# Optimization experiments

Hardware: AMD Instinct MI355X
Metric: run time of the kernel (lower is better)

## Reference

```python
import jax, jax.numpy as jnp
import numpy as np


def setup_inputs() -> dict:
    key = jax.random.key(0)
    k1, k2 = jax.random.split(key)
    B, S, H, D = 4, 2048, 12, 64
    v = jax.random.normal(k1, (B, S, H, D), dtype=jnp.float32)
    # learned per-head positional weights, sorted ascending along last dim
    # (mirrors torch.sort(torch.randn(H, S), dim=-1)[0])
    w = jnp.sort(jax.random.normal(k2, (H, S), dtype=jnp.float32), axis=-1)
    return {"v": v, "w": w}


def reference(v, w):
    # PositionalBias._naive
    # v: [B, S, H, D]; w: [H, S_max]
    B, S, H, D = v.shape
    seq_len = S - 2  # v[:, 1:-1] is the non-special-token span
    w_ = w[:, :seq_len]  # [H, seq_len]
    # _construct_bias builds bias[h, l, j] = w[h, |l - j|] (symmetric Toeplitz)
    pos = jnp.arange(seq_len)
    idx = jnp.abs(pos[:, None] - pos[None, :])  # [seq_len, seq_len]
    bias = w_[:, idx]  # [H, seq_len, seq_len]
    # zero-pad one row/col on each side -> [H, S, S]
    bias = jnp.pad(bias, ((0, 0), (1, 1), (1, 1)))
    # z_pb: [1, S, H]
    z_pb = jnp.sum(bias, axis=-1).T[None, :, :]
    # pbv: [B, S, H, D]
    pbv = jnp.einsum('nlhd,hlj->njhd', v, bias)
    return (pbv, z_pb)
```

## Files before the change

### kernel.cpp

```cpp
#include <hip/hip_runtime.h>
#include <hip/hip_bf16.h>


typedef short short8 __attribute__((ext_vector_type(8)));
typedef float floatx4 __attribute__((ext_vector_type(4)));
typedef unsigned uint4_ __attribute__((ext_vector_type(4)));

#define QN 4352

__device__ __attribute__((aligned(16))) short g_vt[4 * 12 * 64 * 2048];
__device__ __attribute__((aligned(16))) short g_wt[12 * QN * 8];

__device__ __forceinline__ unsigned short f2bf(float f) {
  union { __hip_bfloat16 b; unsigned short u; } cv;
  cv.b = __float2bfloat16(f);
  return cv.u;
}

__global__ __launch_bounds__(256) void prep_kernel(const float* __restrict__ v,
                                                   const float* __restrict__ w,
                                                   float* __restrict__ out) {
  __shared__ unsigned tls[64 * 65];
  __shared__ float zls[4096];
  __shared__ float wsum[4];

  const int bx  = blockIdx.x;
  const int tid = threadIdx.x;

  if (bx >= 780) {
    const int idx = bx - 780;
    const int h = idx >> 4;
    const int c = idx & 15;
    const float* wh = w + (size_t)h * 2048;
    short* F = g_wt + (size_t)h * QN * 8;
    const int qs = c * 272;
    for (int q = qs + tid; q < qs + 272; q += 256) {
      unsigned short buf[8] __attribute__((aligned(16)));
      #pragma unroll
      for (int i = 0; i < 8; ++i) {
        int t = 2174 - q - i;
        int a = t < 0 ? -t : t;
        buf[i] = (a <= 2045) ? f2bf(wh[a]) : (unsigned short)0;
      }
      *(short8*)&F[(size_t)q * 8] = *(const short8*)buf;
    }
    return;
  }

  if (bx >= 768) {
    const int h = bx - 768;
    float* wvv = zls;
    float* pfx = zls + 2048;
    const float* wh = w + (size_t)h * 2048;
    float* zout = out + 6291456;
    for (int i = tid; i < 2048; i += 256) wvv[i] = (i < 2046) ? wh[i] : 0.f;
    __syncthreads();
    const int base = tid * 8;
    float run0 = 0.f;
    #pragma unroll
    for (int k = 0; k < 8; ++k) run0 += wvv[base + k];
    float x = run0;
    #pragma unroll
    for (int dd = 1; dd < 64; dd <<= 1) {
      float y = __shfl_up(x, dd);
      if ((tid & 63) >= dd) x += y;
    }
    if ((tid & 63) == 63) wsum[tid >> 6] = x;
    __syncthreads();
    const int wid4 = tid >> 6;
    float woff = 0.f;
    #pragma unroll
    for (int u = 0; u < 3; ++u) { float t = wsum[u]; if (u < wid4) woff += t; }
    float pr = x + woff - run0;
    #pragma unroll
    for (int k = 0; k < 8; ++k) { pr += wvv[base + k]; pfx[base + k] = pr; }
    __syncthreads();
    for (int i = tid; i < 2046; i += 256) {
      float z = pfx[i] + pfx[2045 - i] - wvv[0];
      zout[(size_t)(i + 1) * 12 + h] = z;
    }
    if (tid == 0) { zout[h] = 0.f; zout[(size_t)2047 * 12 + h] = 0.f; }
    return;
  }

  const int chunk = bx & 15;
  const int slice = bx >> 4;
  const int n = slice / 12, h = slice - n * 12;
  const int lane = tid & 63;
  const int wv   = tid >> 6;
  const int lbase = chunk * 128 + wv * 32;

  const float* src = v + (((size_t)n * 2048 + lbase) * 12 + h) * 64 + lane;
  #pragma unroll
  for (int kk = 0; kk < 16; ++kk) {
    float f0 = src[(size_t)(2 * kk)     * 768];
    float f1 = src[(size_t)(2 * kk + 1) * 768];
    int l = lbase + 2 * kk;
    unsigned lo = (l == 0)        ? 0u : (unsigned)f2bf(f0);
    unsigned hi = (l + 1 == 2047) ? 0u : (unsigned)f2bf(f1);
    tls[lane * 65 + wv * 16 + kk] = lo | (hi << 16);
  }
  __syncthreads();

  const int r = tid >> 2;
  const int m = tid & 3;
  unsigned xbuf[16];
  #pragma unroll
  for (int k = 0; k < 16; ++k) xbuf[k] = tls[r * 65 + m * 16 + k];
  unsigned* dstu = (unsigned*)(g_vt + (((size_t)n * 12 + h) * 64 + r) * 2048 +
                               (size_t)chunk * 128) + m * 16;
  #pragma unroll
  for (int k4 = 0; k4 < 4; ++k4) {
    uint4_ val = {xbuf[k4 * 4], xbuf[k4 * 4 + 1], xbuf[k4 * 4 + 2], xbuf[k4 * 4 + 3]};
    *(uint4_*)&dstu[k4 * 4] = val;
  }
}

__global__ __launch_bounds__(256, 3) void gemm_kernel(float* __restrict__ out) {
  __shared__ __attribute__((aligned(16))) short Als[2304 * 8];

  const int bx  = blockIdx.x;
  const int tid = threadIdx.x;

  const int slice = bx % 48;
  const int jt    = bx / 48;
  const int ndt = slice & 3;
  const int h   = slice >> 2;
  const int lane = tid & 63;
  const int wid  = tid >> 6;
  const int lm = lane & 15, quad = lane >> 4;
  const int jb = jt * 128;
  const int d  = wid * 16 + lm;

  const short* vtb = g_vt + (((size_t)ndt * 12 + h) * 64 + d) * 2048;

  short8 afr[16];
  short8 Bp0[4], Bp1[4];

  Bp0[0] = *(const short8*)&vtb[quad * 8];
  Bp1[0] = *(const short8*)&vtb[quad * 8 + 32];
  Bp0[1] = *(const short8*)&vtb[64 + quad * 8];
  Bp1[1] = *(const short8*)&vtb[64 + quad * 8 + 32];

  const short* wsrc = g_wt + (size_t)h * QN * 8 + (size_t)(2047 - jb) * 8;
  #pragma unroll
  for (int k = 0; k < 9; ++k) {
    *(short8*)&Als[(size_t)(k * 256 + tid) * 8] =
        *(const short8*)&wsrc[(size_t)(k * 256 + tid) * 8];
  }
  __syncthreads();

  const int abase = 127 + quad * 8 - lm;
  unsigned az0 = (unsigned)(unsigned long long)(&Als[0]) + (unsigned)(abase * 16) - 1792u;
  unsigned long long vb0 = (unsigned long long)(const void*)(vtb + quad * 8);

  floatx4 acc[8];
  #pragma unroll
  for (int ma = 0; ma < 8; ++ma) acc[ma] = (floatx4){0.f, 0.f, 0.f, 0.f};

#define A_PRO(D) \
  asm volatile("ds_read_b128 %0, %1 offset:%2" : "=v"(afr[D]) : "v"(az0), "n"(256 * (D)));
  A_PRO(0) A_PRO(1) A_PRO(2) A_PRO(3) A_PRO(4)
  A_PRO(5) A_PRO(6) A_PRO(7) A_PRO(8) A_PRO(9)
#undef A_PRO

#define G_ITER(T)                                                                        \
  {                                                                                      \
    if ((T) < 30) {                                                                      \
      asm volatile("global_load_dwordx4 %0, %1, off offset:%2"                           \
                   : "=v"(Bp0[((T) + 2) & 3])                                            \
                   : "v"(vb0), "n"((((T) < 30 ? (T) + 2 : 0) * 128)));                   \
      asm volatile("global_load_dwordx4 %0, %1, off offset:%2"                           \
                   : "=v"(Bp1[((T) + 2) & 3])                                            \
                   : "v"(vb0), "n"((((T) < 30 ? (T) + 2 : 0) * 128 + 64)));              \
    }                                                                                    \
    if ((T) < 31) {                                                                      \
      asm volatile("ds_read_b128 %0, %1 offset:%2"                                       \
                   : "=v"(afr[(4 * (T) + 10) & 15])                                      \
                   : "v"(az0), "n"(((T) < 31 ? 1024 * (T) + 2560 : 0)));                 \
      asm volatile("ds_read_b128 %0, %1 offset:%2"                                       \
                   : "=v"(afr[(4 * (T) + 11) & 15])                                      \
                   : "v"(az0), "n"(((T) < 31 ? 1024 * (T) + 2816 : 0)));                 \
      asm volatile("ds_read_b128 %0, %1 offset:%2"                                       \
                   : "=v"(afr[(4 * (T) + 12) & 15])                                      \
                   : "v"(az0), "n"(((T) < 31 ? 1024 * (T) + 3072 : 0)));                 \
      asm volatile("ds_read_b128 %0, %1 offset:%2"                                       \
                   : "=v"(afr[(4 * (T) + 13) & 15])                                      \
                   : "v"(az0), "n"(((T) < 31 ? 1024 * (T) + 3328 : 0)));                 \
    }                                                                                    \
    if ((T) < 30)       asm volatile("s_waitcnt vmcnt(4) lgkmcnt(4)" ::: "memory");      \
    else if ((T) == 30) asm volatile("s_waitcnt vmcnt(2) lgkmcnt(4)" ::: "memory");      \
    else                asm volatile("s_waitcnt vmcnt(0) lgkmcnt(0)" ::: "memory");      \
    __builtin_amdgcn_sched_barrier(0);                                                   \
    __builtin_amdgcn_s_setprio(1);                                                       \
    _Pragma("unroll")                                                                    \
    for (int ma = 0; ma < 8; ++ma)                         \
      acc[ma] = __builtin_amdgcn_mfma_f32_16x16x32_bf16(                                 \
          afr[(4 * (T) + 7 - ma) & 15], Bp0[(T) & 3], acc[ma], 0, 0, 0);                 \
    _Pragma("unroll")                                                                    \
    for (int ma = 0; ma < 8; ++ma)                        \
      acc[ma] = __builtin_amdgcn_mfma_f32_16x16x32_bf16(                                 \
          afr[(4 * (T) + 9 - ma) & 15], Bp1[(T) & 3], acc[ma], 0, 0, 0);                 \
    __builtin_amdgcn_s_setprio(0);                                                       \
  }

  G_ITER(0)  G_ITER(1)  G_ITER(2)  G_ITER(3)  G_ITER(4)  G_ITER(5)  G_ITER(6)  G_ITER(7)
  G_ITER(8)  G_ITER(9)  G_ITER(10) G_ITER(11) G_ITER(12) G_ITER(13) G_ITER(14) G_ITER(15)
  G_ITER(16) G_ITER(17) G_ITER(18) G_ITER(19) G_ITER(20) G_ITER(21) G_ITER(22) G_ITER(23)
  G_ITER(24) G_ITER(25) G_ITER(26) G_ITER(27) G_ITER(28) G_ITER(29) G_ITER(30) G_ITER(31)
#undef G_ITER

  float* obase = out + (size_t)ndt * 1572864 + (size_t)h * 64 + d;
  #pragma unroll
  for (int ma = 0; ma < 8; ++ma) {
    floatx4 cc = acc[ma];
    #pragma unroll
    for (int r = 0; r < 4; ++r) {
      int j = jb + ma * 16 + quad * 4 + r;
      float val = (j == 0 || j == 2047) ? 0.f : cc[r];
      obase[(size_t)j * 768] = val;
    }
  }
}

extern "C" void kernel_launch(void* const* d_in, const int* in_sizes, int n_in,
                              void* d_out, int out_size, void* d_ws, size_t ws_size,
                              hipStream_t stream) {
  const float* v = (const float*)d_in[0];
  const float* w = (const float*)d_in[1];
  float* out = (float*)d_out;
  prep_kernel<<<dim3(972), 256, 0, stream>>>(v, w, out);
  gemm_kernel<<<dim3(768), 256, 0, stream>>>(out);
}
```

Measured before the change: 106.7 us.

## Fuse prep and GEMM into one kernel with atomic-counter dependency waits

Merges the transpose/bf16-convert, Toeplitz weight-table build and z_pb prefix-sum stages into the GEMM kernel. Each block does its share of prep work, then spins on global atomic counters until the v-transpose slice and the weight table for its head are complete. The point is to drop the second launch and the gap between kernels, and to let prep overlap with GEMM. In exchange it adds spin-wait synchronisation that relies on all 768 blocks being co-resident (checked via an occupancy query, with the two-kernel path as fallback). It also adds counter-reset logic that must be correct across repeated calls.

```diff
diff --git a/kernel.cpp b/kernel.cpp
--- a/kernel.cpp
+++ b/kernel.cpp
@@ -10,6 +10,10 @@
 
 __device__ __attribute__((aligned(16))) short g_vt[4 * 12 * 64 * 2048];
 __device__ __attribute__((aligned(16))) short g_wt[12 * QN * 8];
+__device__ int vt_cnt[48];
+__device__ int wt_cnt[12];
+__device__ int vt_done[48];
+__device__ int wt_done[12];
 
 __device__ __forceinline__ unsigned short f2bf(float f) {
   union { __hip_bfloat16 b; unsigned short u; } cv;
@@ -17,72 +21,26 @@
   return cv.u;
 }
 
-__global__ __launch_bounds__(256) void prep_kernel(const float* __restrict__ v,
-                                                   const float* __restrict__ w,
-                                                   float* __restrict__ out) {
-  __shared__ unsigned tls[64 * 65];
-  __shared__ float zls[4096];
-  __shared__ float wsum[4];
-
-  const int bx  = blockIdx.x;
-  const int tid = threadIdx.x;
-
-  if (bx >= 780) {
-    const int idx = bx - 780;
-    const int h = idx >> 4;
-    const int c = idx & 15;
-    const float* wh = w + (size_t)h * 2048;
-    short* F = g_wt + (size_t)h * QN * 8;
-    const int qs = c * 272;
-    for (int q = qs + tid; q < qs + 272; q += 256) {
-      unsigned short buf[8] __attribute__((aligned(16)));
-      #pragma unroll
-      for (int i = 0; i < 8; ++i) {
-        int t = 2174 - q - i;
-        int a = t < 0 ? -t : t;
-        buf[i] = (a <= 2045) ? f2bf(wh[a]) : (unsigned short)0;
-      }
-      *(short8*)&F[(size_t)q * 8] = *(const short8*)buf;
+__device__ __forceinline__ void do_gwt(int idx, int tid, const float* __restrict__ w) {
+  const int h = idx >> 4;
+  const int c = idx & 15;
+  const float* wh = w + (size_t)h * 2048;
+  short* F = g_wt + (size_t)h * QN * 8;
+  const int qs = c * 272;
+  for (int q = qs + tid; q < qs + 272; q += 256) {
+    unsigned short buf[8] __attribute__((aligned(16)));
+    #pragma unroll
+    for (int i = 0; i < 8; ++i) {
+      int t = 2174 - q - i;
+      int a = t < 0 ? -t : t;
+      buf[i] = (a <= 2045) ? f2bf(wh[a]) : (unsigned short)0;
     }
-    return;
-  }
-
-  if (bx >= 768) {
-    const int h = bx - 768;
-    float* wvv = zls;
-    float* pfx = zls + 2048;
-    const float* wh = w + (size_t)h * 2048;
-    float* zout = out + 6291456;
-    for (int i = tid; i < 2048; i += 256) wvv[i] = (i < 2046) ? wh[i] : 0.f;
-    __syncthreads();
-    const int base = tid * 8;
-    float run0 = 0.f;
-    #pragma unroll
-    for (int k = 0; k < 8; ++k) run0 += wvv[base + k];
-    float x = run0;
-    #pragma unroll
-    for (int dd = 1; dd < 64; dd <<= 1) {
-      float y = __shfl_up(x, dd);
-      if ((tid & 63) >= dd) x += y;
-    }
-    if ((tid & 63) == 63) wsum[tid >> 6] = x;
-    __syncthreads();
-    const int wid4 = tid >> 6;
-    float woff = 0.f;
-    #pragma unroll
-    for (int u = 0; u < 3; ++u) { float t = wsum[u]; if (u < wid4) woff += t; }
-    float pr = x + woff - run0;
-    #pragma unroll
-    for (int k = 0; k < 8; ++k) { pr += wvv[base + k]; pfx[base + k] = pr; }
-    __syncthreads();
-    for (int i = tid; i < 2046; i += 256) {
-      float z = pfx[i] + pfx[2045 - i] - wvv[0];
-      zout[(size_t)(i + 1) * 12 + h] = z;
-    }
-    if (tid == 0) { zout[h] = 0.f; zout[(size_t)2047 * 12 + h] = 0.f; }
-    return;
-  }
-
+    *(short8*)&F[(size_t)q * 8] = *(const short8*)buf;
+  }
+}
+
+__device__ __forceinline__ void do_transpose(int bx, int tid, unsigned* tls,
+                                             const float* __restrict__ v) {
   const int chunk = bx & 15;
   const int slice = bx >> 4;
   const int n = slice / 12, h = slice - n * 12;
@@ -116,12 +74,43 @@
   }
 }
 
-__global__ __launch_bounds__(256, 3) void gemm_kernel(float* __restrict__ out) {
-  __shared__ __attribute__((aligned(16))) short Als[2304 * 8];
-
-  const int bx  = blockIdx.x;
-  const int tid = threadIdx.x;
-
+__device__ __forceinline__ void do_zpb(int h, int tid, float* zls, float* wsum,
+                                       const float* __restrict__ w,
+                                       float* __restrict__ out) {
+  float* wvv = zls;
+  float* pfx = zls + 2048;
+  const float* wh = w + (size_t)h * 2048;
+  float* zout = out + 6291456;
+  for (int i = tid; i < 2048; i += 256) wvv[i] = (i < 2046) ? wh[i] : 0.f;
+  __syncthreads();
+  const int base = tid * 8;
+  float run0 = 0.f;
+  #pragma unroll
+  for (int k = 0; k < 8; ++k) run0 += wvv[base + k];
+  float x = run0;
+  #pragma unroll
+  for (int dd = 1; dd < 64; dd <<= 1) {
+    float y = __shfl_up(x, dd);
+    if ((tid & 63) >= dd) x += y;
+  }
+  if ((tid & 63) == 63) wsum[tid >> 6] = x;
+  __syncthreads();
+  const int wid4 = tid >> 6;
+  float woff = 0.f;
+  #pragma unroll
+  for (int u = 0; u < 3; ++u) { float t = wsum[u]; if (u < wid4) woff += t; }
+  float pr = x + woff - run0;
+  #pragma unroll
+  for (int k = 0; k < 8; ++k) { pr += wvv[base + k]; pfx[base + k] = pr; }
+  __syncthreads();
+  for (int i = tid; i < 2046; i += 256) {
+    float z = pfx[i] + pfx[2045 - i] - wvv[0];
+    zout[(size_t)(i + 1) * 12 + h] = z;
+  }
+  if (tid == 0) { zout[h] = 0.f; zout[(size_t)2047 * 12 + h] = 0.f; }
+}
+
+__device__ void do_gemm(int bx, int tid, short* Als, float* __restrict__ out) {
   const int slice = bx % 48;
   const int jt    = bx / 48;
   const int ndt = slice & 3;
@@ -223,12 +212,89 @@
   }
 }
 
+__global__ __launch_bounds__(256, 3) void fused_kernel(const float* __restrict__ v,
+                                                       const float* __restrict__ w,
+                                                       float* __restrict__ out) {
+  __shared__ __attribute__((aligned(16))) char smem[36864];
+  const int bx  = blockIdx.x;
+  const int tid = threadIdx.x;
+
+  do_transpose(bx, tid, (unsigned*)smem, v);
+  __threadfence();
+  __syncthreads();
+  if (tid == 0) atomicAdd(&vt_cnt[bx >> 4], 1);
+
+  if (bx < 192) {
+    do_gwt(bx, tid, w);
+    __threadfence();
+    __syncthreads();
+    if (tid == 0) atomicAdd(&wt_cnt[bx >> 4], 1);
+  } else if (bx < 204) {
+    __syncthreads();
+    do_zpb(bx - 192, tid, (float*)smem, (float*)(smem + 16384), w, out);
+  }
+
+  const int slice = bx % 48;
+  const int ndt = slice & 3, h = slice >> 2;
+  const int vts = ndt * 12 + h;
+  if (tid == 0) {
+    while (__hip_atomic_load(&vt_cnt[vts], __ATOMIC_RELAXED, __HIP_MEMORY_SCOPE_AGENT) < 16 ||
+           __hip_atomic_load(&wt_cnt[h],  __ATOMIC_RELAXED, __HIP_MEMORY_SCOPE_AGENT) < 16)
+      __builtin_amdgcn_s_sleep(2);
+  }
+  __syncthreads();
+  __threadfence();
+
+  if (tid == 0) {
+    if (atomicAdd(&vt_done[vts], 1) == 15) {
+      __hip_atomic_store(&vt_cnt[vts], 0, __ATOMIC_RELAXED, __HIP_MEMORY_SCOPE_AGENT);
+      __hip_atomic_store(&vt_done[vts], 0, __ATOMIC_RELAXED, __HIP_MEMORY_SCOPE_AGENT);
+    }
+    if (atomicAdd(&wt_done[h], 1) == 63) {
+      __hip_atomic_store(&wt_cnt[h], 0, __ATOMIC_RELAXED, __HIP_MEMORY_SCOPE_AGENT);
+      __hip_atomic_store(&wt_done[h], 0, __ATOMIC_RELAXED, __HIP_MEMORY_SCOPE_AGENT);
+    }
+  }
+  __syncthreads();
+
+  do_gemm(bx, tid, (short*)smem, out);
+}
+
+__global__ __launch_bounds__(256) void prep_kernel(const float* __restrict__ v,
+                                                   const float* __restrict__ w,
+                                                   float* __restrict__ out) {
+  __shared__ __attribute__((aligned(16))) char smem[36864];
+  const int bx  = blockIdx.x;
+  const int tid = threadIdx.x;
+  if (bx >= 780) { do_gwt(bx - 780, tid, w); return; }
+  if (bx >= 768) { do_zpb(bx - 768, tid, (float*)smem, (float*)(smem + 16384), w, out); return; }
+  do_transpose(bx, tid, (unsigned*)smem, v);
+}
+
+__global__ __launch_bounds__(256, 3) void gemm_kernel(float* __restrict__ out) {
+  __shared__ __attribute__((aligned(16))) char smem[36864];
+  do_gemm(blockIdx.x, threadIdx.x, (short*)smem, out);
+}
+
 extern "C" void kernel_launch(void* const* d_in, const int* in_sizes, int n_in,
                               void* d_out, int out_size, void* d_ws, size_t ws_size,
                               hipStream_t stream) {
   const float* v = (const float*)d_in[0];
   const float* w = (const float*)d_in[1];
   float* out = (float*)d_out;
-  prep_kernel<<<dim3(972), 256, 0, stream>>>(v, w, out);
-  gemm_kernel<<<dim3(768), 256, 0, stream>>>(out);
-}
+
+  static int fused_ok = -1;
+  if (fused_ok < 0) {
+    int nb = 0;
+    if (hipOccupancyMaxActiveBlocksPerMultiprocessor(&nb, fused_kernel, 256, 0) != hipSuccess)
+      nb = 0;
+    fused_ok = (nb >= 3) ? 1 : 0;
+  }
+
+  if (fused_ok) {
+    fused_kernel<<<dim3(768), 256, 0, stream>>>(v, w, out);
+  } else {
+    prep_kernel<<<dim3(972), 256, 0, stream>>>(v, w, out);
+    gemm_kernel<<<dim3(768), 256, 0, stream>>>(out);
+  }
+}
```

Result: slower. 111.6 us (+4.6%).
